# Optimization experiments

Hardware: AMD Instinct MI355X
Metric: run time of the kernel (lower is better)

Reference implementation:

```python
import jax, jax.numpy as jnp
import numpy as np

N_NODES = 50000
N_EDGES = 800000
N_GRAPHS = 64


def setup_inputs() -> dict:
    key = jax.random.key(0)
    ks = jax.random.split(key, 12)

    def w(k, shape):
        fan_in = shape[0]
        return jax.random.normal(k, shape, dtype=jnp.float32) / np.sqrt(fan_in)

    x = jax.random.normal(ks[0], (N_NODES, 6), dtype=jnp.float32)
    edge_index = jax.random.randint(ks[1], (2, N_EDGES), 0, N_NODES, dtype=jnp.int64)
    batch = jnp.sort(jax.random.randint(ks[2], (N_NODES,), 0, N_GRAPHS, dtype=jnp.int64))
    return {
        "x": x,
        "edge_index": edge_index,
        "batch": batch,
        "W_in": w(ks[3], (6, 64)),
        "b_in": jnp.zeros((64,), jnp.float32),
        "W1": w(ks[4], (64, 128)),
        "b1": jnp.zeros((128,), jnp.float32),
        "W2": w(ks[5], (128, 128)),
        "b2": jnp.zeros((128,), jnp.float32),
        "Wp": w(ks[6], (256, 256)),
        "bp": jnp.zeros((256,), jnp.float32),
    }


def reference(x, edge_index, batch, W_in, b_in, W1, b1, W2, b2, Wp, bp):
    n = x.shape[0]
    self_loop = jnp.arange(n, dtype=edge_index.dtype)
    src = jnp.concatenate([edge_index[0], self_loop])  # [E+N]
    dst = jnp.concatenate([edge_index[1], self_loop])
    # GCN symmetric normalization with self-loops (PyG GCNConv default)
    deg = jax.ops.segment_sum(jnp.ones_like(dst, x.dtype), dst, num_segments=n)
    dinv = jax.lax.rsqrt(deg)  # deg >= 1 because of self-loops
    norm = (dinv[src] * dinv[dst])[:, None]  # [E+N, 1]

    def gcn(h, W, b):
        hw = h @ W                       # linear first, like GCNConv
        msg = hw[src] * norm             # gather + normalize per edge
        return jax.ops.segment_sum(msg, dst, num_segments=n) + b

    h = x @ W_in + b_in                  # input_projection
    h = jax.nn.relu(gcn(h, W1, b1))      # relu(gnn1(...))
    h = jax.nn.relu(gcn(h, W2, b2))      # relu(gnn2(...))

    # global mean / max pooling over batch segments
    counts = jax.ops.segment_sum(jnp.ones((n,), h.dtype), batch, num_segments=N_GRAPHS)
    h_mean = jax.ops.segment_sum(h, batch, num_segments=N_GRAPHS) / jnp.maximum(counts, 1.0)[:, None]
    h_max = jax.ops.segment_max(h, batch, num_segments=N_GRAPHS)
    h_max = jnp.where(counts[:, None] > 0, h_max, 0.0)
    h_graph = jnp.concatenate([h_mean, h_max], axis=1)  # [G, 256]

    # projection MLP: Linear + ReLU (Dropout is identity in eval)
    return jax.nn.relu(h_graph @ Wp + bp)
```

## Files before the change

kernel.cpp:

```cpp
#include <hip/hip_runtime.h>
#include <hip/hip_fp16.h>

#define N_NODES 50000
#define N_EDGES 800000
#define N_GRAPHS 64
#define N_PAD 50048

#define CB 256
#define EPB (N_EDGES / CB)
#define NBUCKET ((N_NODES + 255) / 256)

typedef _Float16 f16x8 __attribute__((ext_vector_type(8)));
typedef float f32x4 __attribute__((ext_vector_type(4)));

struct H8 { __half2 a, b, c, d; };


__global__ void k_prep(const float* __restrict__ W1, const float* __restrict__ W2,
                       _Float16* __restrict__ Wt1, _Float16* __restrict__ Wt2,
                       float* psum, float* pmax, int* totals) {
    int idx = blockIdx.x * blockDim.x + threadIdx.x;
    if (idx < 128 * 64) {
        int n = idx >> 6, k = idx & 63;
        Wt1[idx] = (_Float16)W1[k * 128 + n];
    } else if (idx < 128 * 64 + 128 * 128) {
        int j = idx - 128 * 64;
        int n = j >> 7, k = j & 127;
        Wt2[j] = (_Float16)W2[k * 128 + n];
    }
    if (idx < N_GRAPHS * 128) { psum[idx] = 0.f; pmax[idx] = 0.f; }
    if (idx < 256) totals[idx] = 0;
}


__global__ __launch_bounds__(256) void k_coarse_hist(const int* __restrict__ dst,
                                                     int* __restrict__ totals) {
    __shared__ int hist[NBUCKET];
    int t = threadIdx.x, b = blockIdx.x;
    for (int i = t; i < NBUCKET; i += 256) hist[i] = 0;
    __syncthreads();
    int e0 = b * EPB;
    for (int e = e0 + t; e < e0 + EPB; e += 256)
        atomicAdd(&hist[dst[e] >> 8], 1);
    __syncthreads();
    for (int i = t; i < NBUCKET; i += 256)
        if (hist[i] > 0) atomicAdd(&totals[i], hist[i]);
}

__global__ void k_bucket_scan(const int* __restrict__ totals, int* __restrict__ bucket_base,
                              int* __restrict__ gcursor, const int* __restrict__ batch,
                              float* __restrict__ pcnt) {
    __shared__ int sh[256];
    int t = threadIdx.x;
    int v = (t < NBUCKET) ? totals[t] : 0;
    sh[t] = v;
    __syncthreads();
    for (int off = 1; off < 256; off <<= 1) {
        int u = (t >= off) ? sh[t - off] : 0;
        __syncthreads();
        sh[t] += u;
        __syncthreads();
    }
    if (t < NBUCKET) {
        int base = sh[t] - v;
        bucket_base[t] = base;
        gcursor[t] = base;
    }
    if (t == 0) bucket_base[NBUCKET] = N_EDGES;
    if (t <= N_GRAPHS) {
        int lo = 0, hi = N_NODES;
        while (lo < hi) {
            int mid = (lo + hi) >> 1;
            if (batch[mid] < t) lo = mid + 1; else hi = mid;
        }
        sh[t] = lo;
    }
    __syncthreads();
    if (t < N_GRAPHS) pcnt[t] = (float)(sh[t + 1] - sh[t]);
}

__global__ __launch_bounds__(256) void k_coarse_scatter(
        const int* __restrict__ src, const int* __restrict__ dst,
        int* __restrict__ gcursor, unsigned int* __restrict__ esort) {
    __shared__ int cur[NBUCKET];
    int t = threadIdx.x, b = blockIdx.x;
    for (int i = t; i < NBUCKET; i += 256) cur[i] = 0;
    __syncthreads();
    int e0 = b * EPB;
    for (int e = e0 + t; e < e0 + EPB; e += 256)
        atomicAdd(&cur[dst[e] >> 8], 1);
    __syncthreads();
    for (int i = t; i < NBUCKET; i += 256) {
        int cnt = cur[i];
        cur[i] = (cnt > 0) ? atomicAdd(&gcursor[i], cnt) : 0;
    }
    __syncthreads();
    for (int e = e0 + t; e < e0 + EPB; e += 256) {
        int d = dst[e];
        int slot = atomicAdd(&cur[d >> 8], 1);
        esort[slot] = ((unsigned)(d & 255) << 16) | (unsigned)src[e];
    }
}

__global__ __launch_bounds__(256) void k_fine_fill_proj(
        const unsigned int* __restrict__ esort, const int* __restrict__ bucket_base,
        int* __restrict__ col, int* __restrict__ row_ptr, float* __restrict__ dinv,
        const float* __restrict__ x, const float* __restrict__ W_in,
        const float* __restrict__ b_in, _Float16* __restrict__ g0) {
    __shared__ int hist[256];
    __shared__ int sc[256];
    __shared__ int cur[256];
    int t = threadIdx.x, b = blockIdx.x;
    hist[t] = 0;
    __syncthreads();
    int base = bucket_base[b], end = bucket_base[b + 1];
    for (int e = base + t; e < end; e += 256)
        atomicAdd(&hist[(esort[e] >> 16) & 255], 1);
    __syncthreads();
    int v = hist[t];
    sc[t] = v;
    __syncthreads();
    for (int off = 1; off < 256; off <<= 1) {
        int u = (t >= off) ? sc[t - off] : 0;
        __syncthreads();
        sc[t] += u;
        __syncthreads();
    }
    int start = base + sc[t] - v;
    cur[t] = start;
    int node = b * 256 + t;
    float di = rsqrtf((float)(v + 1));
    if (node < N_NODES) {
        row_ptr[node] = start;
        dinv[node] = di;
    }
    if (b == 0 && t == 0) row_ptr[N_NODES] = N_EDGES;
    __syncthreads();
    for (int e = base + t; e < end; e += 256) {
        unsigned pk = esort[e];
        int slot = atomicAdd(&cur[(pk >> 16) & 255], 1);
        col[slot] = (int)(pk & 0xffffu);
    }
    if (node < N_NODES) {
        float xr[6];
#pragma unroll
        for (int k = 0; k < 6; k++) xr[k] = x[node * 6 + k];
#pragma unroll
        for (int oc = 0; oc < 8; oc++) {
            f16x8 o;
#pragma unroll
            for (int j = 0; j < 8; j++) {
                int cl = oc * 8 + j;
                float acc = b_in[cl];
#pragma unroll
                for (int k = 0; k < 6; k++) acc += xr[k] * W_in[k * 64 + cl];
                o[j] = (_Float16)(acc * di);
            }
            *(f16x8*)&g0[(size_t)node * 64 + oc * 8] = o;
        }
    }
}

template <int K, int ROWS, bool HALF_OUT, bool POOL>
__global__ __launch_bounds__(256, 8) void k_gnn(
        const _Float16* __restrict__ g, const int* __restrict__ row_ptr,
        const int* __restrict__ col, const _Float16* __restrict__ Wt_h,
        const float* __restrict__ b, const float* __restrict__ dinv,
        void* __restrict__ outp, const int* __restrict__ batch,
        float* __restrict__ psum, float* __restrict__ pmax, int n) {
    constexpr int KP = K + 8;
    constexpr int TPR = 256 / ROWS;
    constexpr int CO8 = K / 8;
    static_assert(K / TPR == 8, "8 channels per gather thread");
    constexpr int S_BYTES = ROWS * KP * 2;
    constexpr int H_BYTES = POOL ? ROWS * 128 * 4 : 0;
    constexpr int SMEM = S_BYTES > H_BYTES ? S_BYTES : H_BYTES;
    __shared__ __align__(16) char smem[SMEM];
    _Float16* Sl = (_Float16*)smem;
    float* Hs = (float*)smem;
    int t = threadIdx.x;

    {
        int row_local = t / TPR;
        int ck = t % TPR;
        int row = blockIdx.x * ROWS + row_local;
        float accA[8] = {};
        float accB[8] = {};
        const H8* gb = (const H8*)g;
        auto addv = [](float* acc, H8 v) {
            float2 f;
            f = __half22float2(v.a); acc[0] += f.x; acc[1] += f.y;
            f = __half22float2(v.b); acc[2] += f.x; acc[3] += f.y;
            f = __half22float2(v.c); acc[4] += f.x; acc[5] += f.y;
            f = __half22float2(v.d); acc[6] += f.x; acc[7] += f.y;
        };
        if (row < n) {
            addv(accA, gb[(size_t)row * CO8 + ck]);
            int e = row_ptr[row], e1 = row_ptr[row + 1];
            for (; e + 3 < e1; e += 4) {
                int c0 = col[e], c1 = col[e + 1], c2 = col[e + 2], c3 = col[e + 3];
                H8 v0 = gb[(size_t)c0 * CO8 + ck];
                H8 v1 = gb[(size_t)c1 * CO8 + ck];
                H8 v2 = gb[(size_t)c2 * CO8 + ck];
                H8 v3 = gb[(size_t)c3 * CO8 + ck];
                addv(accA, v0);
                addv(accB, v1);
                addv(accA, v2);
                addv(accB, v3);
            }
            if (e + 1 < e1) {
                H8 v0 = gb[(size_t)col[e] * CO8 + ck];
                H8 v1 = gb[(size_t)col[e + 1] * CO8 + ck];
                addv(accA, v0);
                addv(accB, v1);
                e += 2;
            }
            if (e < e1) addv(accA, gb[(size_t)col[e] * CO8 + ck]);
        }
        f16x8 o;
#pragma unroll
        for (int q = 0; q < 8; q++) o[q] = (_Float16)(accA[q] + accB[q]);
        *(f16x8*)&Sl[row_local * KP + ck * 8] = o;
    }
    __syncthreads();

    int wave = t >> 6;
    int lane = t & 63;
    int m = lane & 15;
    int quad = lane >> 4;
    constexpr int COLT = (ROWS == 16) ? 2 : 4;
    int col_base = (ROWS == 16) ? wave * 32 : (wave >> 1) * 64;
    int rbl = (ROWS == 16) ? 0 : (wave & 1) * 16;
    int wrow0 = blockIdx.x * ROWS + rbl;

    f32x4 acc[COLT] = {};
#pragma unroll
    for (int k0 = 0; k0 < K; k0 += 32) {
        f16x8 a = *(const f16x8*)&Sl[(rbl + m) * KP + k0 + quad * 8];
#pragma unroll
        for (int ct = 0; ct < COLT; ct++) {
            f16x8 bw = *(const f16x8*)(Wt_h + (size_t)(col_base + ct * 16 + m) * K + k0 + quad * 8);
            acc[ct] = __builtin_amdgcn_mfma_f32_16x16x32_f16(a, bw, acc[ct], 0, 0, 0);
        }
    }

    if (!POOL) {
#pragma unroll
        for (int r = 0; r < 4; r++) {
            int row = wrow0 + quad * 4 + r;
            if (row < n) {
                float di = dinv[row];
#pragma unroll
                for (int ct = 0; ct < COLT; ct++) {
                    int colb = col_base + ct * 16 + m;
                    float v = fmaxf(di * acc[ct][r] + b[colb], 0.f);
                    if (HALF_OUT)
                        ((_Float16*)outp)[(size_t)row * 128 + colb] = (_Float16)(v * di);
                    else
                        ((float*)outp)[(size_t)row * 128 + colb] = v;
                }
            }
        }
    } else {
        __syncthreads();
#pragma unroll
        for (int r = 0; r < 4; r++) {
            int rl = quad * 4 + r;
            int row = wrow0 + rl;
            float di = (row < n) ? dinv[row] : 0.f;
#pragma unroll
            for (int ct = 0; ct < COLT; ct++) {
                int colb = col_base + ct * 16 + m;
                float v = fmaxf(di * acc[ct][r] + b[colb], 0.f);
                Hs[rl * 128 + colb] = (row < n) ? v : 0.f;
            }
        }
        __syncthreads();
        if (t < 128) {
            int colb = t;
            int row0b = blockIdx.x * ROWS;
            float s = 0.f, mx = 0.f;
            int gcur = batch[row0b < n ? row0b : (n - 1)];
            for (int rl = 0; rl < ROWS; rl++) {
                int row = row0b + rl;
                if (row >= n) break;
                int gi = batch[row];
                if (gi != gcur) {
                    atomicAdd(&psum[gcur * 128 + colb], s);
                    atomicMax((int*)&pmax[gcur * 128 + colb], __float_as_int(mx));
                    s = 0.f; mx = 0.f; gcur = gi;
                }
                float v = Hs[rl * 128 + colb];
                s += v;
                mx = fmaxf(mx, v);
            }
            atomicAdd(&psum[gcur * 128 + colb], s);
            atomicMax((int*)&pmax[gcur * 128 + colb], __float_as_int(mx));
        }
    }
}


__global__ void k_final(const float* __restrict__ psum, const float* __restrict__ pmax,
                        const float* __restrict__ pcnt, const float* __restrict__ Wp,
                        const float* __restrict__ bp, float* __restrict__ out) {
    int t = blockIdx.x * blockDim.x + threadIdx.x;
    if (t >= N_GRAPHS * 256) return;
    int g = t >> 8, j = t & 255;
    float inv = 1.0f / fmaxf(pcnt[g], 1.0f);
    float acc = bp[j];
#pragma unroll 4
    for (int k = 0; k < 128; k++) acc += (psum[g * 128 + k] * inv) * Wp[k * 256 + j];
#pragma unroll 4
    for (int k = 0; k < 128; k++) acc += pmax[g * 128 + k] * Wp[(128 + k) * 256 + j];
    out[t] = fmaxf(acc, 0.f);
}

extern "C" void kernel_launch(void* const* d_in, const int* in_sizes, int n_in,
                              void* d_out, int out_size, void* d_ws, size_t ws_size,
                              hipStream_t stream) {
    const int N = N_NODES, E = N_EDGES;
    const float* x    = (const float*)d_in[0];
    const int*   ei   = (const int*)d_in[1];
    const int*   src  = ei;
    const int*   dst  = ei + E;
    const int*   batch= (const int*)d_in[2];
    const float* W_in = (const float*)d_in[3];
    const float* b_in = (const float*)d_in[4];
    const float* W1   = (const float*)d_in[5];
    const float* b1   = (const float*)d_in[6];
    const float* W2   = (const float*)d_in[7];
    const float* b2   = (const float*)d_in[8];
    const float* Wp   = (const float*)d_in[9];
    const float* bp   = (const float*)d_in[10];
    float* out = (float*)d_out;

    char* p = (char*)d_ws;
    int* totals      = (int*)p;   p += 256 * 4;
    int* bucket_base = (int*)p;   p += 256 * 4;
    int* gcursor     = (int*)p;   p += 256 * 4;
    int* row_ptr     = (int*)p;   p += (N_PAD + 64) * 4;
    int* col         = (int*)p;   p += (size_t)N_EDGES * 4;
    unsigned* esort  = (unsigned*)p; p += (size_t)N_EDGES * 4;
    float* dinv      = (float*)p; p += N_PAD * 4;
    _Float16* Wt1    = (_Float16*)p; p += 128 * 64 * 2;
    _Float16* Wt2    = (_Float16*)p; p += 128 * 128 * 2;
    _Float16* g0h    = (_Float16*)p; p += (size_t)N_PAD * 64 * 2;
    _Float16* g1h    = (_Float16*)p; p += (size_t)N_PAD * 128 * 2;
    float* psum      = (float*)p; p += N_GRAPHS * 128 * 4;
    float* pmax      = (float*)p; p += N_GRAPHS * 128 * 4;
    float* pcnt      = (float*)p;

    const int TB = 256;
    dim3 blk(TB);

    k_prep<<<(128 * 64 + 128 * 128 + TB - 1) / TB, blk, 0, stream>>>(
        W1, W2, Wt1, Wt2, psum, pmax, totals);

    k_coarse_hist<<<CB, blk, 0, stream>>>(dst, totals);
    k_bucket_scan<<<1, blk, 0, stream>>>(totals, bucket_base, gcursor, batch, pcnt);
    k_coarse_scatter<<<CB, blk, 0, stream>>>(src, dst, gcursor, esort);
    k_fine_fill_proj<<<NBUCKET, blk, 0, stream>>>(esort, bucket_base, col, row_ptr, dinv,
                                                  x, W_in, b_in, g0h);

    k_gnn<64, 32, true, false><<<(N + 31) / 32, blk, 0, stream>>>(
        g0h, row_ptr, col, Wt1, b1, dinv, g1h, nullptr, nullptr, nullptr, N);

    k_gnn<128, 16, false, true><<<(N + 15) / 16, blk, 0, stream>>>(
        g1h, row_ptr, col, Wt2, b2, dinv, nullptr, batch, psum, pmax, N);

    k_final<<<(N_GRAPHS * 256 + TB - 1) / TB, blk, 0, stream>>>(psum, pmax, pcnt, Wp, bp, out);
}
```

Before: 206.5 us.

## Replace global-atomic bucket cursors with per-block count table and LDS-staged fine fill

```diff
diff --git a/kernel.cpp b/kernel.cpp
--- a/kernel.cpp
+++ b/kernel.cpp
@@ -9,6 +9,7 @@
 #define CB 256
 #define EPB (N_EDGES / CB)
 #define NBUCKET ((N_NODES + 255) / 256)
+#define ECAP 6144
 
 typedef _Float16 f16x8 __attribute__((ext_vector_type(8)));
 typedef float f32x4 __attribute__((ext_vector_type(4)));
@@ -16,44 +17,47 @@
 struct H8 { __half2 a, b, c, d; };
 
 
-__global__ void k_prep(const float* __restrict__ W1, const float* __restrict__ W2,
-                       _Float16* __restrict__ Wt1, _Float16* __restrict__ Wt2,
-                       float* psum, float* pmax, int* totals) {
-    int idx = blockIdx.x * blockDim.x + threadIdx.x;
-    if (idx < 128 * 64) {
-        int n = idx >> 6, k = idx & 63;
-        Wt1[idx] = (_Float16)W1[k * 128 + n];
-    } else if (idx < 128 * 64 + 128 * 128) {
-        int j = idx - 128 * 64;
+__global__ __launch_bounds__(256) void k_hist_prep(
+        const int* __restrict__ dst, int* __restrict__ counts,
+        const float* __restrict__ W1, const float* __restrict__ W2,
+        _Float16* __restrict__ Wt1, _Float16* __restrict__ Wt2,
+        float* __restrict__ psum, float* __restrict__ pmax) {
+    __shared__ int hist[256];
+    int t = threadIdx.x, b = blockIdx.x;
+    hist[t] = 0;
+    int gid = b * 256 + t;
+    if (gid < 128 * 64) {
+        int n = gid >> 6, k = gid & 63;
+        Wt1[gid] = (_Float16)W1[k * 128 + n];
+    } else if (gid < 128 * 64 + 128 * 128) {
+        int j = gid - 128 * 64;
         int n = j >> 7, k = j & 127;
         Wt2[j] = (_Float16)W2[k * 128 + n];
     }
-    if (idx < N_GRAPHS * 128) { psum[idx] = 0.f; pmax[idx] = 0.f; }
-    if (idx < 256) totals[idx] = 0;
-}
-
-
-__global__ __launch_bounds__(256) void k_coarse_hist(const int* __restrict__ dst,
-                                                     int* __restrict__ totals) {
-    __shared__ int hist[NBUCKET];
-    int t = threadIdx.x, b = blockIdx.x;
-    for (int i = t; i < NBUCKET; i += 256) hist[i] = 0;
+    if (gid < N_GRAPHS * 128) { psum[gid] = 0.f; pmax[gid] = 0.f; }
     __syncthreads();
     int e0 = b * EPB;
     for (int e = e0 + t; e < e0 + EPB; e += 256)
         atomicAdd(&hist[dst[e] >> 8], 1);
     __syncthreads();
     for (int i = t; i < NBUCKET; i += 256)
-        if (hist[i] > 0) atomicAdd(&totals[i], hist[i]);
-}
-
-__global__ void k_bucket_scan(const int* __restrict__ totals, int* __restrict__ bucket_base,
-                              int* __restrict__ gcursor, const int* __restrict__ batch,
-                              float* __restrict__ pcnt) {
+        counts[i * CB + b] = hist[i];
+}
+
+
+__global__ __launch_bounds__(256) void k_scan(
+        const int* __restrict__ counts, int* __restrict__ cbase,
+        int* __restrict__ bucket_base, const int* __restrict__ batch,
+        float* __restrict__ pcnt) {
     __shared__ int sh[256];
+    __shared__ int lb[N_GRAPHS + 1];
     int t = threadIdx.x;
-    int v = (t < NBUCKET) ? totals[t] : 0;
-    sh[t] = v;
+    int tot = 0;
+    if (t < NBUCKET) {
+#pragma unroll 8
+        for (int b = 0; b < CB; b++) tot += counts[t * CB + b];
+    }
+    sh[t] = tot;
     __syncthreads();
     for (int off = 1; off < 256; off <<= 1) {
         int u = (t >= off) ? sh[t - off] : 0;
@@ -61,10 +65,16 @@
         sh[t] += u;
         __syncthreads();
     }
+    int base = sh[t] - tot;
     if (t < NBUCKET) {
-        int base = sh[t] - v;
         bucket_base[t] = base;
-        gcursor[t] = base;
+        int run = base;
+#pragma unroll 4
+        for (int b = 0; b < CB; b++) {
+            int c = counts[t * CB + b];
+            cbase[t * CB + b] = run;
+            run += c;
+        }
     }
     if (t == 0) bucket_base[NBUCKET] = N_EDGES;
     if (t <= N_GRAPHS) {
@@ -73,28 +83,21 @@
             int mid = (lo + hi) >> 1;
             if (batch[mid] < t) lo = mid + 1; else hi = mid;
         }
-        sh[t] = lo;
-    }
-    __syncthreads();
-    if (t < N_GRAPHS) pcnt[t] = (float)(sh[t + 1] - sh[t]);
-}
-
-__global__ __launch_bounds__(256) void k_coarse_scatter(
+        lb[t] = lo;
+    }
+    __syncthreads();
+    if (t < N_GRAPHS) pcnt[t] = (float)(lb[t + 1] - lb[t]);
+}
+
+
+__global__ __launch_bounds__(256) void k_scatter(
         const int* __restrict__ src, const int* __restrict__ dst,
-        int* __restrict__ gcursor, unsigned int* __restrict__ esort) {
+        const int* __restrict__ cbase, unsigned int* __restrict__ esort) {
     __shared__ int cur[NBUCKET];
     int t = threadIdx.x, b = blockIdx.x;
-    for (int i = t; i < NBUCKET; i += 256) cur[i] = 0;
+    for (int i = t; i < NBUCKET; i += 256) cur[i] = cbase[i * CB + b];
     __syncthreads();
     int e0 = b * EPB;
-    for (int e = e0 + t; e < e0 + EPB; e += 256)
-        atomicAdd(&cur[dst[e] >> 8], 1);
-    __syncthreads();
-    for (int i = t; i < NBUCKET; i += 256) {
-        int cnt = cur[i];
-        cur[i] = (cnt > 0) ? atomicAdd(&gcursor[i], cnt) : 0;
-    }
-    __syncthreads();
     for (int e = e0 + t; e < e0 + EPB; e += 256) {
         int d = dst[e];
         int slot = atomicAdd(&cur[d >> 8], 1);
@@ -110,12 +113,20 @@
     __shared__ int hist[256];
     __shared__ int sc[256];
     __shared__ int cur[256];
+    __shared__ unsigned es[ECAP];
     int t = threadIdx.x, b = blockIdx.x;
     hist[t] = 0;
     __syncthreads();
     int base = bucket_base[b], end = bucket_base[b + 1];
-    for (int e = base + t; e < end; e += 256)
-        atomicAdd(&hist[(esort[e] >> 16) & 255], 1);
+    int cnt = end - base;
+    int stg = cnt < ECAP ? cnt : ECAP;
+    for (int i = t; i < stg; i += 256) {
+        unsigned pk = esort[base + i];
+        es[i] = pk;
+        atomicAdd(&hist[(pk >> 16) & 255], 1);
+    }
+    for (int i = ECAP + t; i < cnt; i += 256)
+        atomicAdd(&hist[(esort[base + i] >> 16) & 255], 1);
     __syncthreads();
     int v = hist[t];
     sc[t] = v;
@@ -136,8 +147,13 @@
     }
     if (b == 0 && t == 0) row_ptr[N_NODES] = N_EDGES;
     __syncthreads();
-    for (int e = base + t; e < end; e += 256) {
-        unsigned pk = esort[e];
+    for (int i = t; i < stg; i += 256) {
+        unsigned pk = es[i];
+        int slot = atomicAdd(&cur[(pk >> 16) & 255], 1);
+        col[slot] = (int)(pk & 0xffffu);
+    }
+    for (int i = ECAP + t; i < cnt; i += 256) {
+        unsigned pk = esort[base + i];
         int slot = atomicAdd(&cur[(pk >> 16) & 255], 1);
         col[slot] = (int)(pk & 0xffffu);
     }
@@ -336,9 +352,9 @@
     float* out = (float*)d_out;
 
     char* p = (char*)d_ws;
-    int* totals      = (int*)p;   p += 256 * 4;
+    int* counts      = (int*)p;   p += NBUCKET * CB * 4;
+    int* cbase       = (int*)p;   p += NBUCKET * CB * 4;
     int* bucket_base = (int*)p;   p += 256 * 4;
-    int* gcursor     = (int*)p;   p += 256 * 4;
     int* row_ptr     = (int*)p;   p += (N_PAD + 64) * 4;
     int* col         = (int*)p;   p += (size_t)N_EDGES * 4;
     unsigned* esort  = (unsigned*)p; p += (size_t)N_EDGES * 4;
@@ -354,12 +370,9 @@
     const int TB = 256;
     dim3 blk(TB);
 
-    k_prep<<<(128 * 64 + 128 * 128 + TB - 1) / TB, blk, 0, stream>>>(
-        W1, W2, Wt1, Wt2, psum, pmax, totals);
-
-    k_coarse_hist<<<CB, blk, 0, stream>>>(dst, totals);
-    k_bucket_scan<<<1, blk, 0, stream>>>(totals, bucket_base, gcursor, batch, pcnt);
-    k_coarse_scatter<<<CB, blk, 0, stream>>>(src, dst, gcursor, esort);
+    k_hist_prep<<<CB, blk, 0, stream>>>(dst, counts, W1, W2, Wt1, Wt2, psum, pmax);
+    k_scan<<<1, blk, 0, stream>>>(counts, cbase, bucket_base, batch, pcnt);
+    k_scatter<<<CB, blk, 0, stream>>>(src, dst, cbase, esort);
     k_fine_fill_proj<<<NBUCKET, blk, 0, stream>>>(esort, bucket_base, col, row_ptr, dinv,
                                                   x, W_in, b_in, g0h);
 
```

Result: slower. 217.9 us (+5.5%).
